# Optimization experiments

Hardware: AMD Instinct MI355X
Metric: run time of the kernel (lower is better)

Reference implementation:

```python
import jax, jax.numpy as jnp
import numpy as np

KH, KW = 3, 3
PAD = 1


def setup_inputs() -> dict:
    key = jax.random.key(0)
    k1, k2 = jax.random.split(key)
    B, C, H, W = 8, 3, 544, 960
    x = jax.random.normal(k1, (B, C, H, W), dtype=jnp.float32)
    filt = jax.random.uniform(k2, (B, C * KH * KW, H, W), dtype=jnp.float32)
    return {"x": x, "filter": filt}


def _local_expand(x):
    # x: [B, C, H, W] -> [B, C*KH*KW, H, W], channel-major ordering (c slowest)
    B, C, H, W = x.shape
    xp = jnp.pad(x, ((0, 0), (0, 0), (PAD, PAD), (PAD, PAD)))
    patches = jnp.stack(
        [xp[:, :, i:i + H, j:j + W] for i in range(KH) for j in range(KW)],
        axis=2,
    )  # [B, C, KH*KW, H, W]
    return patches.reshape(B, C * KH * KW, H, W)


def reference(x, filter):
    x_le = _local_expand(x)                      # [B, C*k^2, H, W]
    out = jnp.sum(x_le * filter, axis=1, keepdims=True)  # [B, 1, H, W]
    return out
```

## Files before the change

kernel.cpp:

```cpp
#include <hip/hip_runtime.h>

constexpr int B = 8, C = 3, H = 544, W = 960;
constexpr int KH = 3, KW = 3;
constexpr int HW = H * W;
constexpr int WQ = W / 4;
constexpr int NK = C * KH * KW;

__global__ __launch_bounds__(256) void DynFilter_kernel(
    const float* __restrict__ x,
    const float* __restrict__ filt,
    float* __restrict__ out)
{
    int tid = blockIdx.x * blockDim.x + threadIdx.x;
    constexpr int total = B * H * WQ;
    if (tid >= total) return;

    int wq = tid % WQ;
    int t  = tid / WQ;
    int h  = t % H;
    int b  = t / H;
    int w0 = wq * 4;

    float4 acc = make_float4(0.f, 0.f, 0.f, 0.f);

    const float* fbase = filt + (size_t)b * NK * HW + (size_t)h * W + w0;

    #pragma unroll
    for (int c = 0; c < C; ++c) {
        const float* xc = x + ((size_t)b * C + c) * HW;
        #pragma unroll
        for (int i = 0; i < KH; ++i) {
            int hr = h + i - 1;
            bool vh = (unsigned)hr < (unsigned)H;
            float xv0, xv1, xv2, xv3, xv4, xv5;
            if (vh) {
                const float* xr = xc + (size_t)hr * W + w0;
                float4 m = *reinterpret_cast<const float4*>(xr);
                xv1 = m.x; xv2 = m.y; xv3 = m.z; xv4 = m.w;
                xv0 = (w0 > 0)      ? xr[-1] : 0.f;
                xv5 = (w0 + 4 < W)  ? xr[4]  : 0.f;
            } else {
                xv0 = xv1 = xv2 = xv3 = xv4 = xv5 = 0.f;
            }
            float xv[6] = {xv0, xv1, xv2, xv3, xv4, xv5};
            #pragma unroll
            for (int j = 0; j < KW; ++j) {
                int k = c * (KH * KW) + i * KW + j;
                float4 f = *reinterpret_cast<const float4*>(fbase + (size_t)k * HW);
                acc.x += xv[j]     * f.x;
                acc.y += xv[j + 1] * f.y;
                acc.z += xv[j + 2] * f.z;
                acc.w += xv[j + 3] * f.w;
            }
        }
    }

    *reinterpret_cast<float4*>(out + (size_t)b * HW + (size_t)h * W + w0) = acc;
}

extern "C" void kernel_launch(void* const* d_in, const int* in_sizes, int n_in,
                              void* d_out, int out_size, void* d_ws, size_t ws_size,
                              hipStream_t stream) {
    const float* x    = (const float*)d_in[0];
    const float* filt = (const float*)d_in[1];
    float* out        = (float*)d_out;

    constexpr int total  = B * H * WQ;
    constexpr int block  = 256;
    constexpr int blocks = (total + block - 1) / block;

    DynFilter_kernel<<<blocks, block, 0, stream>>>(x, filt, out);
}
```

Before: 101.2 us.

## Process eight pixels per thread and swizzle block order across XCDs

Each thread now computes eight output pixels instead of four, issuing two float4 loads per filter plane and reusing the loaded x row across more outputs. Block indices are remapped so that consecutive hardware blocks (round-robined across XCDs) map to contiguous chunks of the image, aiming for better L2 locality per XCD. The grid is made exact, which removes the bounds check. The trade-off is higher register use and fewer threads in flight for a memory-bound kernel dominated by streaming the filter tensor.

```diff
diff --git a/kernel.cpp b/kernel.cpp
--- a/kernel.cpp
+++ b/kernel.cpp
@@ -3,25 +3,32 @@
 constexpr int B = 8, C = 3, H = 544, W = 960;
 constexpr int KH = 3, KW = 3;
 constexpr int HW = H * W;
-constexpr int WQ = W / 4;
+constexpr int WT = 8;
+constexpr int WQ = W / WT;
 constexpr int NK = C * KH * KW;
+constexpr int BLOCK = 256;
+constexpr int TOTAL = B * H * WQ;
+constexpr int NBLK = TOTAL / BLOCK;
+static_assert(TOTAL % BLOCK == 0, "grid must be exact");
+static_assert(NBLK % 8 == 0, "swizzle must be bijective");
 
-__global__ __launch_bounds__(256) void DynFilter_kernel(
+__global__ __launch_bounds__(BLOCK) void DynFilter_kernel(
     const float* __restrict__ x,
     const float* __restrict__ filt,
     float* __restrict__ out)
 {
-    int tid = blockIdx.x * blockDim.x + threadIdx.x;
-    constexpr int total = B * H * WQ;
-    if (tid >= total) return;
+    int bid  = (int)blockIdx.x;
+    int sbid = (bid & 7) * (NBLK / 8) + (bid >> 3);
+    int tid  = sbid * BLOCK + (int)threadIdx.x;
 
     int wq = tid % WQ;
     int t  = tid / WQ;
     int h  = t % H;
     int b  = t / H;
-    int w0 = wq * 4;
+    int w0 = wq * WT;
 
-    float4 acc = make_float4(0.f, 0.f, 0.f, 0.f);
+    float4 acc0 = make_float4(0.f, 0.f, 0.f, 0.f);
+    float4 acc1 = make_float4(0.f, 0.f, 0.f, 0.f);
 
     const float* fbase = filt + (size_t)b * NK * HW + (size_t)h * W + w0;
 
@@ -32,30 +39,40 @@
         for (int i = 0; i < KH; ++i) {
             int hr = h + i - 1;
             bool vh = (unsigned)hr < (unsigned)H;
-            float xv0, xv1, xv2, xv3, xv4, xv5;
+            float xv[WT + 2];
             if (vh) {
                 const float* xr = xc + (size_t)hr * W + w0;
-                float4 m = *reinterpret_cast<const float4*>(xr);
-                xv1 = m.x; xv2 = m.y; xv3 = m.z; xv4 = m.w;
-                xv0 = (w0 > 0)      ? xr[-1] : 0.f;
-                xv5 = (w0 + 4 < W)  ? xr[4]  : 0.f;
+                float4 m0 = *reinterpret_cast<const float4*>(xr);
+                float4 m1 = *reinterpret_cast<const float4*>(xr + 4);
+                xv[1] = m0.x; xv[2] = m0.y; xv[3] = m0.z; xv[4] = m0.w;
+                xv[5] = m1.x; xv[6] = m1.y; xv[7] = m1.z; xv[8] = m1.w;
+                xv[0] = (w0 > 0)      ? xr[-1] : 0.f;
+                xv[9] = (w0 + WT < W) ? xr[WT] : 0.f;
             } else {
-                xv0 = xv1 = xv2 = xv3 = xv4 = xv5 = 0.f;
+                #pragma unroll
+                for (int q = 0; q < WT + 2; ++q) xv[q] = 0.f;
             }
-            float xv[6] = {xv0, xv1, xv2, xv3, xv4, xv5};
             #pragma unroll
             for (int j = 0; j < KW; ++j) {
                 int k = c * (KH * KW) + i * KW + j;
-                float4 f = *reinterpret_cast<const float4*>(fbase + (size_t)k * HW);
-                acc.x += xv[j]     * f.x;
-                acc.y += xv[j + 1] * f.y;
-                acc.z += xv[j + 2] * f.z;
-                acc.w += xv[j + 3] * f.w;
+                const float* fp = fbase + (size_t)k * HW;
+                float4 f0 = *reinterpret_cast<const float4*>(fp);
+                float4 f1 = *reinterpret_cast<const float4*>(fp + 4);
+                acc0.x += xv[j]     * f0.x;
+                acc0.y += xv[j + 1] * f0.y;
+                acc0.z += xv[j + 2] * f0.z;
+                acc0.w += xv[j + 3] * f0.w;
+                acc1.x += xv[j + 4] * f1.x;
+                acc1.y += xv[j + 5] * f1.y;
+                acc1.z += xv[j + 6] * f1.z;
+                acc1.w += xv[j + 7] * f1.w;
             }
         }
     }
 
-    *reinterpret_cast<float4*>(out + (size_t)b * HW + (size_t)h * W + w0) = acc;
+    float* op = out + (size_t)b * HW + (size_t)h * W + w0;
+    *reinterpret_cast<float4*>(op)     = acc0;
+    *reinterpret_cast<float4*>(op + 4) = acc1;
 }
 
 extern "C" void kernel_launch(void* const* d_in, const int* in_sizes, int n_in,
@@ -65,9 +82,5 @@
     const float* filt = (const float*)d_in[1];
     float* out        = (float*)d_out;
 
-    constexpr int total  = B * H * WQ;
-    constexpr int block  = 256;
-    constexpr int blocks = (total + block - 1) / block;
-
-    DynFilter_kernel<<<blocks, block, 0, stream>>>(x, filt, out);
+    DynFilter_kernel<<<NBLK, BLOCK, 0, stream>>>(x, filt, out);
 }
```

After: 101.6 us. Within noise of the previous version (+0.4%).
